# Kernel tuning notes

Hardware: AMD Instinct MI355X
Metric: run time of the kernel (lower is better)

## Reference

```python
import jax, jax.numpy as jnp
import numpy as np
import math

N_HEADS = 16
EPS = 1e-6


def rmsnorm(x, w):
    xf = x.astype(jnp.float32)
    n = xf * jax.lax.rsqrt(jnp.mean(xf * xf, axis=-1, keepdims=True) + EPS)
    return n.astype(x.dtype) * w


def setup_inputs() -> dict:
    key = jax.random.key(0)
    ks = jax.random.split(key, 8)
    B, T, C, Hf = 1, 4096, 1024, 4096
    s = lambda fan_in: 1.0 / math.sqrt(fan_in)
    return {
        "x": jax.random.normal(ks[0], (B, T, C), jnp.float32),
        "attn_norm_w": jnp.ones((C,), jnp.float32),
        "ffn_norm_w": jnp.ones((C,), jnp.float32),
        "c_attn_w": jax.random.normal(ks[1], (3 * C, C), jnp.float32) * s(C),
        "c_proj_w": jax.random.normal(ks[2], (C, C), jnp.float32) * s(C),
        "w1": jax.random.normal(ks[3], (Hf, C), jnp.float32) * s(C),
        "w2": jax.random.normal(ks[4], (C, Hf), jnp.float32) * s(Hf),
        "w3": jax.random.normal(ks[5], (Hf, C), jnp.float32) * s(C),
    }


def attention(x, c_attn_w, c_proj_w):
    B, T, C = x.shape
    hd = C // N_HEADS
    qkv = x @ c_attn_w.T  # [B,T,3C]
    q, k, v = jnp.split(qkv, 3, axis=-1)
    q = q.reshape(B, T, N_HEADS, hd).transpose(0, 2, 1, 3)  # [B,H,T,hd]
    k = k.reshape(B, T, N_HEADS, hd).transpose(0, 2, 1, 3)
    v = v.reshape(B, T, N_HEADS, hd).transpose(0, 2, 1, 3)
    att = jnp.einsum('bhqd,bhkd->bhqk', q, k) * (1.0 / math.sqrt(hd))
    mask = jnp.tril(jnp.ones((T, T), bool))  # causal
    att = jnp.where(mask, att, -jnp.inf)
    att = jax.nn.softmax(att, axis=-1)
    y = jnp.einsum('bhqk,bhkd->bhqd', att, v)
    y = y.transpose(0, 2, 1, 3).reshape(B, T, C)
    return y @ c_proj_w.T


def ffn(x, w1, w2, w3):
    return (jax.nn.silu(x @ w1.T) * (x @ w3.T)) @ w2.T


def reference(x, attn_norm_w, ffn_norm_w, c_attn_w, c_proj_w, w1, w2, w3):
    x = x + attention(rmsnorm(x, attn_norm_w), c_attn_w, c_proj_w)
    x = x + ffn(rmsnorm(x, ffn_norm_w), w1, w2, w3)
    return x
```

## Files before the change

kernel.cpp:

```cpp
#include <hip/hip_runtime.h>
#include <hip/hip_bf16.h>

typedef __hip_bfloat16 bf16;
typedef __bf16 bf16r;
typedef bf16r bf16x8 __attribute__((ext_vector_type(8)));
typedef bf16r bf16x4 __attribute__((ext_vector_type(4)));
typedef float f32x4 __attribute__((ext_vector_type(4)));

#define T_SEQ 4096
#define C_DIM 1024
#define LD_QKV 3072
#define MB(x) ((size_t)(x) << 20)
#define SCL 0.18033688011112042f

static __device__ __forceinline__ unsigned short f2bf(float f) {
    bf16 h = (bf16)f;
    return *reinterpret_cast<unsigned short*>(&h);
}

__global__ __launch_bounds__(256) void cvt_w(const float* __restrict__ src, size_t eoff,
                                             ushort4* __restrict__ dst, int n4) {
    int i = blockIdx.x * 256 + threadIdx.x;
    const int stride = gridDim.x * 256;
    const float4* s = (const float4*)(src + eoff);
    for (; i < n4; i += stride) {
        float4 v = s[i];
        ushort4 o;
        o.x = f2bf(v.x); o.y = f2bf(v.y); o.z = f2bf(v.z); o.w = f2bf(v.w);
        dst[i] = o;
    }
}

__global__ __launch_bounds__(256) void cvt_w2h(const float* __restrict__ src, int coff,
                                               ushort4* __restrict__ dst) {
    const int i = blockIdx.x * 256 + threadIdx.x;
    const int row = i >> 9;
    const int c4 = i & 511;
    float4 v = *(const float4*)(src + (size_t)row * 4096 + coff + c4 * 4);
    ushort4 o;
    o.x = f2bf(v.x); o.y = f2bf(v.y); o.z = f2bf(v.z); o.w = f2bf(v.w);
    dst[i] = o;
}

__global__ __launch_bounds__(256) void rmsnorm_k(const float* __restrict__ x,
                                                 const float* __restrict__ w,
                                                 bf16* __restrict__ out) {
    const int row = blockIdx.x;
    const int tid = threadIdx.x;
    const float* xr = x + (size_t)row * C_DIM;
    float v[4];
    float ss = 0.f;
#pragma unroll
    for (int i = 0; i < 4; i++) { v[i] = xr[tid * 4 + i]; ss += v[i] * v[i]; }
#pragma unroll
    for (int off = 32; off; off >>= 1) ss += __shfl_xor(ss, off);
    __shared__ float red[4];
    if ((tid & 63) == 0) red[tid >> 6] = ss;
    __syncthreads();
    const float tot = red[0] + red[1] + red[2] + red[3];
    const float scale = rsqrtf(tot * (1.0f / C_DIM) + 1e-6f);
#pragma unroll
    for (int i = 0; i < 4; i++) {
        const int c = tid * 4 + i;
        out[(size_t)row * C_DIM + c] = (bf16)(v[i] * scale * w[c]);
    }
}

template <int RESID, int OUTF32>
__global__ __launch_bounds__(256) void gemm128(const bf16* __restrict__ A, int lda,
                                               const bf16* __restrict__ B, int ldb,
                                               const void* __restrict__ resid,
                                               void* __restrict__ out,
                                               int N, int K) {
    __shared__ __align__(16) bf16r As[128 * 32];
    __shared__ __align__(16) bf16r Bs[128 * 32];
    const int tid = threadIdx.x;
    const int w = tid >> 6, lane = tid & 63;
    const int c = lane & 15, qd = lane >> 4;
    const int wm = w >> 1, wn = w & 1;
    const int mbase = blockIdx.y * 128;
    const int nbase = blockIdx.x * 128;

    const int srow = lane >> 2, schk = lane & 3;
    const bf16* gA = A + (size_t)(mbase + w * 32 + srow) * lda + schk * 8;
    const bf16* gB = B + (size_t)(nbase + w * 32 + srow) * ldb + schk * 8;

    f32x4 acc[4][4] = {};

    for (int k0 = 0; k0 < K; k0 += 32) {
        __syncthreads();
#pragma unroll
        for (int s = 0; s < 2; s++) {
            __builtin_amdgcn_global_load_lds(
                (const __attribute__((address_space(1))) void*)(gA + (size_t)(s * 16) * lda + k0),
                (__attribute__((address_space(3))) void*)&As[(w * 32 + s * 16) * 32], 16, 0, 0);
            __builtin_amdgcn_global_load_lds(
                (const __attribute__((address_space(1))) void*)(gB + (size_t)(s * 16) * ldb + k0),
                (__attribute__((address_space(3))) void*)&Bs[(w * 32 + s * 16) * 32], 16, 0, 0);
        }
        __syncthreads();

        bf16x8 a[4], b[4];
#pragma unroll
        for (int i = 0; i < 4; i++)
            a[i] = *(const bf16x8*)&As[(wm * 64 + i * 16 + c) * 32 + qd * 8];
#pragma unroll
        for (int j = 0; j < 4; j++)
            b[j] = *(const bf16x8*)&Bs[(wn * 64 + j * 16 + c) * 32 + qd * 8];
#pragma unroll
        for (int i = 0; i < 4; i++)
#pragma unroll
            for (int j = 0; j < 4; j++)
                acc[i][j] = __builtin_amdgcn_mfma_f32_16x16x32_bf16(a[i], b[j], acc[i][j], 0, 0, 0);
    }

#pragma unroll
    for (int i = 0; i < 4; i++) {
#pragma unroll
        for (int j = 0; j < 4; j++) {
            const int col = nbase + wn * 64 + j * 16 + c;
#pragma unroll
            for (int reg = 0; reg < 4; reg++) {
                const int row = mbase + wm * 64 + i * 16 + qd * 4 + reg;
                const size_t idx = (size_t)row * N + col;
                float v = acc[i][j][reg];
                if (RESID == 2) v += ((const float*)resid)[idx];
                if (RESID == 3) {
                    const float a1 = (float)((const bf16*)resid)[idx];
                    v = (a1 / (1.0f + __expf(-a1))) * v;
                }
                if (OUTF32)
                    ((float*)out)[idx] = v;
                else
                    ((bf16*)out)[idx] = (bf16)v;
            }
        }
    }
}

__global__ __launch_bounds__(256) void build_tr(const bf16* __restrict__ qkv,
                                                bf16* __restrict__ dst, int soff) {
    const int h = blockIdx.y;
    const int tb = blockIdx.x;
    __shared__ bf16 tile[64][65];
    const int tx = threadIdx.x & 63;
    const int ty = threadIdx.x >> 6;
    for (int rr = ty; rr < 64; rr += 4)
        tile[rr][tx] = qkv[(size_t)(tb * 64 + rr) * LD_QKV + soff + h * 64 + tx];
    __syncthreads();
    for (int rr = ty; rr < 64; rr += 4)
        dst[((size_t)h * 64 + rr) * T_SEQ + tb * 64 + tx] = tile[tx][rr];
}

#define CTR_STRIDE 16
__global__ void zero_ctr(int* p) { if (threadIdx.x < 8 * CTR_STRIDE) p[threadIdx.x] = 0; }

__global__ __launch_bounds__(256) void attn_mfma(const bf16* __restrict__ qkv,
                                                 const bf16* __restrict__ VT,
                                                 bf16* __restrict__ y,
                                                 int* __restrict__ ctrs) {
    __shared__ __align__(16) bf16r Ks[128][64];
    __shared__ __align__(16) bf16r VTs[64][128];
    __shared__ __align__(16) bf16r Ps[4][16][128];
    __shared__ int s_wi;

    const int tid  = threadIdx.x;
    const int w    = tid >> 6;
    const int lane = tid & 63;
    const int c    = lane & 15;
    const int qd   = lane >> 4;
    const int sw   = c & 7;
    const int qi   = blockIdx.x & 7;
    int* ctr = ctrs + qi * CTR_STRIDE;

    while (true) {
        __syncthreads();
        if (tid == 0) s_wi = atomicAdd(ctr, 1);
        __syncthreads();
        const int j = s_wi;
        if (j >= 128) break;

        const int h    = qi + 8 * (j & 1);
        const int qb   = 63 - (j >> 1);
        const int qrow = qb * 64 + w * 16 + c;

        bf16x8 qf[2];
        {
            const bf16* qp = qkv + (size_t)qrow * LD_QKV + h * 64;
            qf[0] = *(const bf16x8*)(qp + qd * 8);
            qf[1] = *(const bf16x8*)(qp + 32 + qd * 8);
        }

        f32x4 O[4] = {};
        float m_i = -1e30f, l_i = 0.f;
        const int nkb = (qb >> 1) + 1;

        for (int kb = 0; kb < nkb; kb++) {
            __syncthreads();
#pragma unroll
            for (int ii = 0; ii < 4; ii++) {
                const int i = ii * 256 + tid;
                const int kr = i >> 3, ch = i & 7;
                *(bf16x8*)&Ks[kr][(ch ^ (kr & 7)) * 8] =
                    *(const bf16x8*)(qkv + (size_t)(kb * 128 + kr) * LD_QKV + C_DIM + h * 64 + ch * 8);
                const int vr = i >> 4, vch = i & 15;
                *(bf16x8*)&VTs[vr][(vch ^ (vr & 7)) * 8] =
                    *(const bf16x8*)(VT + ((size_t)h * 64 + vr) * T_SEQ + kb * 128 + vch * 8);
            }
            __syncthreads();

            f32x4 ST[8];
#pragma unroll
            for (int kt = 0; kt < 8; kt++) {
                f32x4 z = {};
#pragma unroll
                for (int ks = 0; ks < 2; ks++) {
                    bf16x8 kf = *(const bf16x8*)&Ks[kt * 16 + c][((ks * 4 + qd) ^ sw) * 8];
                    z = __builtin_amdgcn_mfma_f32_16x16x32_bf16(kf, qf[ks], z, 0, 0, 0);
                }
                ST[kt] = z;
            }

            if (kb == nkb - 1) {
#pragma unroll
                for (int kt = 0; kt < 8; kt++)
#pragma unroll
                    for (int r = 0; r < 4; r++) {
                        float s = ST[kt][r] * SCL;
                        if (kb * 128 + kt * 16 + qd * 4 + r > qrow) s = -1e30f;
                        ST[kt][r] = s;
                    }
            } else {
#pragma unroll
                for (int kt = 0; kt < 8; kt++)
#pragma unroll
                    for (int r = 0; r < 4; r++) ST[kt][r] *= SCL;
            }

            float mb = -1e30f;
#pragma unroll
            for (int kt = 0; kt < 8; kt++)
#pragma unroll
                for (int r = 0; r < 4; r++) mb = fmaxf(mb, ST[kt][r]);
            mb = fmaxf(mb, __shfl_xor(mb, 16));
            mb = fmaxf(mb, __shfl_xor(mb, 32));

            bf16x4 pv[8];
            float rs = 0.f;
            if (__all(mb - m_i <= 8.0f)) {
#pragma unroll
                for (int kt = 0; kt < 8; kt++)
#pragma unroll
                    for (int r = 0; r < 4; r++) {
                        const float p = exp2f(ST[kt][r] - m_i);
                        pv[kt][r] = (bf16r)p;
                        rs += p;
                    }
                rs += __shfl_xor(rs, 16);
                rs += __shfl_xor(rs, 32);
                l_i += rs;
            } else {
                const float mnew = fmaxf(m_i, mb);
                const float alpha = exp2f(m_i - mnew);
#pragma unroll
                for (int kt = 0; kt < 8; kt++)
#pragma unroll
                    for (int r = 0; r < 4; r++) {
                        const float p = exp2f(ST[kt][r] - mnew);
                        pv[kt][r] = (bf16r)p;
                        rs += p;
                    }
                rs += __shfl_xor(rs, 16);
                rs += __shfl_xor(rs, 32);
                l_i = l_i * alpha + rs;
                m_i = mnew;
#pragma unroll
                for (int dt = 0; dt < 4; dt++)
#pragma unroll
                    for (int r = 0; r < 4; r++) O[dt][r] *= alpha;
            }

#pragma unroll
            for (int kt = 0; kt < 8; kt++) {
                const int phys = (kt * 2 + (qd >> 1)) ^ sw;
                *(bf16x4*)&Ps[w][c][phys * 8 + (qd & 1) * 4] = pv[kt];
            }

#pragma unroll
            for (int ks = 0; ks < 4; ks++) {
                bf16x8 pf = *(const bf16x8*)&Ps[w][c][((ks * 4 + qd) ^ sw) * 8];
#pragma unroll
                for (int dt = 0; dt < 4; dt++) {
                    bf16x8 vf = *(const bf16x8*)&VTs[dt * 16 + c][((ks * 4 + qd) ^ sw) * 8];
                    O[dt] = __builtin_amdgcn_mfma_f32_16x16x32_bf16(vf, pf, O[dt], 0, 0, 0);
                }
            }
        }

        const float inv_l = 1.0f / l_i;
#pragma unroll
        for (int dt = 0; dt < 4; dt++) {
            bf16x4 ov;
#pragma unroll
            for (int r = 0; r < 4; r++) ov[r] = (bf16r)(O[dt][r] * inv_l);
            *(bf16x4*)(y + (size_t)qrow * C_DIM + h * 64 + dt * 16 + qd * 4) = ov;
        }
    }
}

extern "C" void kernel_launch(void* const* d_in, const int* in_sizes, int n_in,
                              void* d_out, int out_size, void* d_ws, size_t ws_size,
                              hipStream_t stream) {
    const float* x        = (const float*)d_in[0];
    const float* attn_w   = (const float*)d_in[1];
    const float* ffn_w    = (const float*)d_in[2];
    const float* c_attn_w = (const float*)d_in[3];
    const float* c_proj_w = (const float*)d_in[4];
    const float* w1       = (const float*)d_in[5];
    const float* w2       = (const float*)d_in[6];
    const float* w3       = (const float*)d_in[7];
    float* xmid = (float*)d_out;

    char* ws = (char*)d_ws;
    bf16* cwA = (bf16*)(ws);
    bf16* cwP = (bf16*)(ws + MB(6));
    bf16* rms = (bf16*)(ws + MB(8));
    bf16* qkv = (bf16*)(ws + MB(16));
    bf16* VT  = (bf16*)(ws + MB(40));
    bf16* y   = (bf16*)(ws + MB(48));
    bf16* w1h = (bf16*)(ws + MB(16));
    bf16* w3h = (bf16*)(ws + MB(20));
    bf16* w2h = (bf16*)(ws + MB(24));
    bf16* h1h = (bf16*)(ws + MB(28));
    int* ctrs = (int*)(ws + MB(8));

    cvt_w<<<512, 256, 0, stream>>>(c_attn_w, 0, (ushort4*)cwA, 3072 * 1024 / 4);
    cvt_w<<<512, 256, 0, stream>>>(c_proj_w, 0, (ushort4*)cwP, 1024 * 1024 / 4);
    rmsnorm_k<<<T_SEQ, 256, 0, stream>>>(x, attn_w, rms);
    gemm128<0, 0><<<dim3(24, 32), 256, 0, stream>>>(rms, C_DIM, cwA, C_DIM, nullptr, qkv, 3072, 1024);
    build_tr<<<dim3(64, 16), 256, 0, stream>>>(qkv, VT, 2 * C_DIM);
    zero_ctr<<<1, 128, 0, stream>>>(ctrs);
    attn_mfma<<<768, 256, 0, stream>>>(qkv, VT, y, ctrs);
    gemm128<2, 1><<<dim3(8, 32), 256, 0, stream>>>(y, C_DIM, cwP, C_DIM, x, xmid, 1024, 1024);
    rmsnorm_k<<<T_SEQ, 256, 0, stream>>>(xmid, ffn_w, rms);
    for (int hh = 0; hh < 2; hh++) {
        cvt_w<<<512, 256, 0, stream>>>(w1, (size_t)hh * 2048 * 1024, (ushort4*)w1h, 2048 * 1024 / 4);
        gemm128<0, 0><<<dim3(16, 32), 256, 0, stream>>>(rms, C_DIM, w1h, C_DIM, nullptr, h1h, 2048, 1024);
        cvt_w<<<512, 256, 0, stream>>>(w3, (size_t)hh * 2048 * 1024, (ushort4*)w3h, 2048 * 1024 / 4);
        gemm128<3, 0><<<dim3(16, 32), 256, 0, stream>>>(rms, C_DIM, w3h, C_DIM, h1h, h1h, 2048, 1024);
        cvt_w2h<<<2048, 256, 0, stream>>>(w2, hh * 2048, (ushort4*)w2h);
        gemm128<2, 1><<<dim3(8, 32), 256, 0, stream>>>(h1h, 2048, w2h, 2048, xmid, xmid, 1024, 2048);
    }
}
```

Before: 531.5 us.

## Fuse W1/W3 GEMMs, fold softmax scale into Q weights, split-K atomics for projections

Adds a gemm_w13 kernel that computes both FFN up-projections in one pass and applies SiLU-gating in its epilogue. This removes the intermediate h1 write/read and one GEMM launch. The softmax scale is folded into the Q rows of the converted attention weight, which drops a multiply from the attention inner loop. The c_proj and w2 GEMMs become split-K over two z-slices using float atomicAdd into xmid, pre-initialized by a copy of x, to raise parallelism on small grids. The cost is extra atomics, a copy pass, higher register pressure in the fused kernel, and nondeterministic summation order.

```diff
diff --git a/kernel.cpp b/kernel.cpp
--- a/kernel.cpp
+++ b/kernel.cpp
@@ -19,14 +19,16 @@
 }
 
 __global__ __launch_bounds__(256) void cvt_w(const float* __restrict__ src, size_t eoff,
-                                             ushort4* __restrict__ dst, int n4) {
+                                             ushort4* __restrict__ dst, int n4,
+                                             int n4scl, float scl) {
     int i = blockIdx.x * 256 + threadIdx.x;
     const int stride = gridDim.x * 256;
     const float4* s = (const float4*)(src + eoff);
     for (; i < n4; i += stride) {
         float4 v = s[i];
+        const float m = (i < n4scl) ? scl : 1.0f;
         ushort4 o;
-        o.x = f2bf(v.x); o.y = f2bf(v.y); o.z = f2bf(v.z); o.w = f2bf(v.w);
+        o.x = f2bf(v.x * m); o.y = f2bf(v.y * m); o.z = f2bf(v.z * m); o.w = f2bf(v.w * m);
         dst[i] = o;
     }
 }
@@ -40,6 +42,13 @@
     ushort4 o;
     o.x = f2bf(v.x); o.y = f2bf(v.y); o.z = f2bf(v.z); o.w = f2bf(v.w);
     dst[i] = o;
+}
+
+__global__ __launch_bounds__(256) void copy_f32(const float4* __restrict__ src,
+                                                float4* __restrict__ dst, int n4) {
+    int i = blockIdx.x * 256 + threadIdx.x;
+    const int stride = gridDim.x * 256;
+    for (; i < n4; i += stride) dst[i] = src[i];
 }
 
 __global__ __launch_bounds__(256) void rmsnorm_k(const float* __restrict__ x,
@@ -80,10 +89,11 @@
     const int wm = w >> 1, wn = w & 1;
     const int mbase = blockIdx.y * 128;
     const int nbase = blockIdx.x * 128;
+    const size_t koff = (size_t)blockIdx.z * K;
 
     const int srow = lane >> 2, schk = lane & 3;
-    const bf16* gA = A + (size_t)(mbase + w * 32 + srow) * lda + schk * 8;
-    const bf16* gB = B + (size_t)(nbase + w * 32 + srow) * ldb + schk * 8;
+    const bf16* gA = A + (size_t)(mbase + w * 32 + srow) * lda + schk * 8 + koff;
+    const bf16* gB = B + (size_t)(nbase + w * 32 + srow) * ldb + schk * 8 + koff;
 
     f32x4 acc[4][4] = {};
 
@@ -129,10 +139,86 @@
                     const float a1 = (float)((const bf16*)resid)[idx];
                     v = (a1 / (1.0f + __expf(-a1))) * v;
                 }
-                if (OUTF32)
+                if (RESID == 4) {
+                    atomicAdd(&((float*)out)[idx], v);
+                } else if (OUTF32) {
                     ((float*)out)[idx] = v;
-                else
+                } else {
                     ((bf16*)out)[idx] = (bf16)v;
+                }
+            }
+        }
+    }
+}
+
+__global__ __launch_bounds__(256, 2) void gemm_w13(const bf16* __restrict__ A,
+                                                   const bf16* __restrict__ B1,
+                                                   const bf16* __restrict__ B3,
+                                                   bf16* __restrict__ out,
+                                                   int N, int K) {
+    __shared__ __align__(16) bf16r As[128 * 32];
+    __shared__ __align__(16) bf16r B1s[128 * 32];
+    __shared__ __align__(16) bf16r B3s[128 * 32];
+    const int tid = threadIdx.x;
+    const int w = tid >> 6, lane = tid & 63;
+    const int c = lane & 15, qd = lane >> 4;
+    const int wm = w >> 1, wn = w & 1;
+    const int mbase = blockIdx.y * 128;
+    const int nbase = blockIdx.x * 128;
+
+    const int srow = lane >> 2, schk = lane & 3;
+    const bf16* gA = A + (size_t)(mbase + w * 32 + srow) * K + schk * 8;
+    const bf16* gB1 = B1 + (size_t)(nbase + w * 32 + srow) * K + schk * 8;
+    const bf16* gB3 = B3 + (size_t)(nbase + w * 32 + srow) * K + schk * 8;
+
+    f32x4 acc1[4][4] = {};
+    f32x4 acc3[4][4] = {};
+
+    for (int k0 = 0; k0 < K; k0 += 32) {
+        __syncthreads();
+#pragma unroll
+        for (int s = 0; s < 2; s++) {
+            __builtin_amdgcn_global_load_lds(
+                (const __attribute__((address_space(1))) void*)(gA + (size_t)(s * 16) * K + k0),
+                (__attribute__((address_space(3))) void*)&As[(w * 32 + s * 16) * 32], 16, 0, 0);
+            __builtin_amdgcn_global_load_lds(
+                (const __attribute__((address_space(1))) void*)(gB1 + (size_t)(s * 16) * K + k0),
+                (__attribute__((address_space(3))) void*)&B1s[(w * 32 + s * 16) * 32], 16, 0, 0);
+            __builtin_amdgcn_global_load_lds(
+                (const __attribute__((address_space(1))) void*)(gB3 + (size_t)(s * 16) * K + k0),
+                (__attribute__((address_space(3))) void*)&B3s[(w * 32 + s * 16) * 32], 16, 0, 0);
+        }
+        __syncthreads();
+
+        bf16x8 a[4], b1[4], b3[4];
+#pragma unroll
+        for (int i = 0; i < 4; i++)
+            a[i] = *(const bf16x8*)&As[(wm * 64 + i * 16 + c) * 32 + qd * 8];
+#pragma unroll
+        for (int j = 0; j < 4; j++) {
+            b1[j] = *(const bf16x8*)&B1s[(wn * 64 + j * 16 + c) * 32 + qd * 8];
+            b3[j] = *(const bf16x8*)&B3s[(wn * 64 + j * 16 + c) * 32 + qd * 8];
+        }
+#pragma unroll
+        for (int i = 0; i < 4; i++)
+#pragma unroll
+            for (int j = 0; j < 4; j++) {
+                acc1[i][j] = __builtin_amdgcn_mfma_f32_16x16x32_bf16(a[i], b1[j], acc1[i][j], 0, 0, 0);
+                acc3[i][j] = __builtin_amdgcn_mfma_f32_16x16x32_bf16(a[i], b3[j], acc3[i][j], 0, 0, 0);
+            }
+    }
+
+#pragma unroll
+    for (int i = 0; i < 4; i++) {
+#pragma unroll
+        for (int j = 0; j < 4; j++) {
+            const int col = nbase + wn * 64 + j * 16 + c;
+#pragma unroll
+            for (int reg = 0; reg < 4; reg++) {
+                const int row = mbase + wm * 64 + i * 16 + qd * 4 + reg;
+                const float a1 = acc1[i][j][reg];
+                const float h = (a1 / (1.0f + __expf(-a1))) * acc3[i][j][reg];
+                out[(size_t)row * N + col] = (bf16)h;
             }
         }
     }
@@ -225,16 +311,8 @@
 #pragma unroll
                 for (int kt = 0; kt < 8; kt++)
 #pragma unroll
-                    for (int r = 0; r < 4; r++) {
-                        float s = ST[kt][r] * SCL;
-                        if (kb * 128 + kt * 16 + qd * 4 + r > qrow) s = -1e30f;
-                        ST[kt][r] = s;
-                    }
-            } else {
-#pragma unroll
-                for (int kt = 0; kt < 8; kt++)
-#pragma unroll
-                    for (int r = 0; r < 4; r++) ST[kt][r] *= SCL;
+                    for (int r = 0; r < 4; r++)
+                        if (kb * 128 + kt * 16 + qd * 4 + r > qrow) ST[kt][r] = -1e30f;
             }
 
             float mb = -1e30f;
@@ -334,21 +412,24 @@
     bf16* h1h = (bf16*)(ws + MB(28));
     int* ctrs = (int*)(ws + MB(8));
 
-    cvt_w<<<512, 256, 0, stream>>>(c_attn_w, 0, (ushort4*)cwA, 3072 * 1024 / 4);
-    cvt_w<<<512, 256, 0, stream>>>(c_proj_w, 0, (ushort4*)cwP, 1024 * 1024 / 4);
+    cvt_w<<<512, 256, 0, stream>>>(c_attn_w, 0, (ushort4*)cwA, 3072 * 1024 / 4,
+                                   1024 * 1024 / 4, SCL);
+    cvt_w<<<512, 256, 0, stream>>>(c_proj_w, 0, (ushort4*)cwP, 1024 * 1024 / 4, 0, 1.0f);
     rmsnorm_k<<<T_SEQ, 256, 0, stream>>>(x, attn_w, rms);
     gemm128<0, 0><<<dim3(24, 32), 256, 0, stream>>>(rms, C_DIM, cwA, C_DIM, nullptr, qkv, 3072, 1024);
     build_tr<<<dim3(64, 16), 256, 0, stream>>>(qkv, VT, 2 * C_DIM);
     zero_ctr<<<1, 128, 0, stream>>>(ctrs);
     attn_mfma<<<768, 256, 0, stream>>>(qkv, VT, y, ctrs);
-    gemm128<2, 1><<<dim3(8, 32), 256, 0, stream>>>(y, C_DIM, cwP, C_DIM, x, xmid, 1024, 1024);
+    copy_f32<<<2048, 256, 0, stream>>>((const float4*)x, (float4*)xmid, T_SEQ * C_DIM / 4);
+    gemm128<4, 1><<<dim3(8, 32, 2), 256, 0, stream>>>(y, C_DIM, cwP, C_DIM, nullptr, xmid, 1024, 512);
     rmsnorm_k<<<T_SEQ, 256, 0, stream>>>(xmid, ffn_w, rms);
     for (int hh = 0; hh < 2; hh++) {
-        cvt_w<<<512, 256, 0, stream>>>(w1, (size_t)hh * 2048 * 1024, (ushort4*)w1h, 2048 * 1024 / 4);
-        gemm128<0, 0><<<dim3(16, 32), 256, 0, stream>>>(rms, C_DIM, w1h, C_DIM, nullptr, h1h, 2048, 1024);
-        cvt_w<<<512, 256, 0, stream>>>(w3, (size_t)hh * 2048 * 1024, (ushort4*)w3h, 2048 * 1024 / 4);
-        gemm128<3, 0><<<dim3(16, 32), 256, 0, stream>>>(rms, C_DIM, w3h, C_DIM, h1h, h1h, 2048, 1024);
+        cvt_w<<<512, 256, 0, stream>>>(w1, (size_t)hh * 2048 * 1024, (ushort4*)w1h,
+                                       2048 * 1024 / 4, 0, 1.0f);
+        cvt_w<<<512, 256, 0, stream>>>(w3, (size_t)hh * 2048 * 1024, (ushort4*)w3h,
+                                       2048 * 1024 / 4, 0, 1.0f);
+        gemm_w13<<<dim3(16, 32), 256, 0, stream>>>(rms, w1h, w3h, h1h, 2048, 1024);
         cvt_w2h<<<2048, 256, 0, stream>>>(w2, hh * 2048, (ushort4*)w2h);
-        gemm128<2, 1><<<dim3(8, 32), 256, 0, stream>>>(h1h, 2048, w2h, 2048, xmid, xmid, 1024, 2048);
-    }
-}
+        gemm128<4, 1><<<dim3(8, 32, 2), 256, 0, stream>>>(h1h, 2048, w2h, 2048, nullptr, xmid, 1024, 1024);
+    }
+}
```

Result: faster. 508.7 us (-4.3%).
